# Optimization experiments

Hardware: AMD Instinct MI355X
Metric: run time of the kernel (lower is better)

The kernel has to match this reference:

```python
import math
import jax, jax.numpy as jnp
import numpy as np

B, C, T = 4, 512, 1024
H = 8
KC = C // H
WIN = 4


def _get_relative_embeddings(emb, length):
    win = (emb.shape[1] - 1) // 2
    pad_length = max(length - (win + 1), 0)
    slice_start = max(win + 1 - length, 0)
    slice_end = slice_start + 2 * length - 1
    if pad_length > 0:
        emb = jnp.pad(emb, ((0, 0), (pad_length, pad_length), (0, 0)))
    return emb[:, slice_start:slice_end]


def _relative_to_absolute(x):
    # x: [b, h, L, 2L-1] -> [b, h, L, L] via skew trick
    b, h, L, _ = x.shape
    x = jnp.pad(x, ((0, 0), (0, 0), (0, 0), (0, 1)))          # [b,h,L,2L]
    x_flat = x.reshape(b, h, L * 2 * L)
    x_flat = jnp.pad(x_flat, ((0, 0), (0, 0), (0, L - 1)))    # [b,h,(L+1)(2L-1)]
    x_final = x_flat.reshape(b, h, L + 1, 2 * L - 1)
    return x_final[:, :, :L, L - 1:]


def _absolute_to_relative(x):
    # x: [b, h, L, L] -> [b, h, L, 2L-1]
    b, h, L, _ = x.shape
    x = jnp.pad(x, ((0, 0), (0, 0), (0, 0), (0, L - 1)))      # [b,h,L,2L-1]
    x_flat = x.reshape(b, h, L * (2 * L - 1))
    x_flat = jnp.pad(x_flat, ((0, 0), (0, 0), (L, 0)))        # [b,h,2L^2]
    x_final = x_flat.reshape(b, h, L, 2 * L)
    return x_final[:, :, :, 1:]


def setup_inputs() -> dict:
    key = jax.random.key(0)
    ks = jax.random.split(key, 12)
    xavier = math.sqrt(6.0 / (C + C))  # xavier_uniform for [C, C, 1] conv weight
    rel_std = KC ** (-0.5)
    return {
        "x": jax.random.normal(ks[0], (B, C, T), dtype=jnp.float32),
        "wq": jax.random.uniform(ks[1], (C, C), jnp.float32, -xavier, xavier),
        "bq": jnp.zeros((C,), jnp.float32),
        "wk": jax.random.uniform(ks[2], (C, C), jnp.float32, -xavier, xavier),
        "bk": jnp.zeros((C,), jnp.float32),
        "wv": jax.random.uniform(ks[3], (C, C), jnp.float32, -xavier, xavier),
        "bv": jnp.zeros((C,), jnp.float32),
        "wo": jax.random.normal(ks[4], (C, C), jnp.float32) * (1.0 / math.sqrt(C)),
        "bo": jnp.zeros((C,), jnp.float32),
        "emb_rel_k": jax.random.normal(ks[5], (1, 2 * WIN + 1, KC), jnp.float32) * rel_std,
        "emb_rel_v": jax.random.normal(ks[6], (1, 2 * WIN + 1, KC), jnp.float32) * rel_std,
    }


def reference(x, wq, bq, wk, bk, wv, bv, wo, bo, emb_rel_k, emb_rel_v):
    b, c, t = x.shape
    # 1x1 conv == channel matmul
    q = jnp.einsum("oi,bit->bot", wq, x) + bq[:, None]
    k = jnp.einsum("oi,bit->bot", wk, x) + bk[:, None]
    v = jnp.einsum("oi,bit->bot", wv, x) + bv[:, None]
    # [b, H, t, kc]
    q = q.reshape(b, H, KC, t).transpose(0, 1, 3, 2)
    k = k.reshape(b, H, KC, t).transpose(0, 1, 3, 2)
    v = v.reshape(b, H, KC, t).transpose(0, 1, 3, 2)
    inv_sqrt = 1.0 / math.sqrt(KC)
    scores = jnp.einsum("bhtc,bhsc->bhts", q, k) * inv_sqrt
    rel_k = _get_relative_embeddings(emb_rel_k, t)[0]            # [2t-1, kc]
    rel_logits = jnp.einsum("bhtc,rc->bhtr", q, rel_k)           # [b,h,t,2t-1]
    scores = scores + _relative_to_absolute(rel_logits) * inv_sqrt
    p_attn = jax.nn.softmax(scores, axis=-1)
    output = jnp.einsum("bhts,bhsc->bhtc", p_attn, v)
    rel_weights = _absolute_to_relative(p_attn)                  # [b,h,t,2t-1]
    rel_v = _get_relative_embeddings(emb_rel_v, t)[0]            # [2t-1, kc]
    output = output + jnp.einsum("bhtr,rc->bhtc", rel_weights, rel_v)
    output = output.transpose(0, 1, 3, 2).reshape(b, c, t)
    return jnp.einsum("oi,bit->bot", wo, output) + bo[:, None]
```

## Files before the change

### kernel.cpp

```cpp
#include <hip/hip_runtime.h>
#include <hip/hip_bf16.h>

#define Bdim 4
#define Cdim 512
#define Tdim 1024
#define Hn   8
#define KCd  64

#define QK_SCALE 0.18033688011112042f

typedef __attribute__((ext_vector_type(8))) short bf16x8;
typedef __attribute__((ext_vector_type(4))) float f32x4;

__device__ __forceinline__ unsigned short f2bf(float f) {
    __hip_bfloat16 h = __float2bfloat16(f);
    return *reinterpret_cast<unsigned short*>(&h);
}
__device__ __forceinline__ float bf16_f32(unsigned short h) {
    return __uint_as_float(((unsigned)h) << 16);
}
__device__ __forceinline__ void split8(const float* f, bf16x8& h8, bf16x8& l8) {
    #pragma unroll
    for (int e = 0; e < 8; ++e) {
        const unsigned short hh = f2bf(f[e]);
        h8[e] = (short)hh;
        l8[e] = (short)f2bf(f[e] - bf16_f32(hh));
    }
}
__device__ __forceinline__ float max3f(float a, float b, float c) {
    return fmaxf(fmaxf(a, b), c);
}

__device__ __forceinline__ int sw(int row, int col) {
    return (row << 6) + ((((col >> 3) ^ (row & 7)) << 3) | (col & 7));
}
__device__ __forceinline__ bf16x8 fragld(const unsigned short* a, int row, int kstep, int quad) {
    return *(const bf16x8*)&a[(row << 6) + ((((kstep << 2) | quad) ^ (row & 7)) << 3)];
}


__global__ __launch_bounds__(256) void prep_kernel(
    const float* __restrict__ wq, const float* __restrict__ wk,
    const float* __restrict__ wv, const float* __restrict__ wo,
    const float* __restrict__ x,
    unsigned short* __restrict__ WAhi, unsigned short* __restrict__ WAlo,
    unsigned short* __restrict__ XBhi, unsigned short* __restrict__ XBlo)
{
    const int w = threadIdx.x >> 6, lane = threadIdx.x & 63;
    const int l15 = lane & 15, quad = lane >> 4;
    const int task = blockIdx.x * 4 + w;

    if (task < 2048) {
        const int mtile = task >> 4, kt = task & 15;
        const int sel = mtile >> 5;
        const float* W = sel == 0 ? wq : (sel == 1 ? wk : (sel == 2 ? wv : wo));
        const int row = (mtile & 31) * 16 + l15;
        const float* p = W + (size_t)row * Cdim + kt * 32 + quad * 8;
        float f[8];
        *(float4*)&f[0] = *(const float4*)p;
        *(float4*)&f[4] = *(const float4*)(p + 4);
        bf16x8 h8, l8;
        split8(f, h8, l8);
        const size_t base = (size_t)task * 512 + lane * 8;
        *(bf16x8*)(WAhi + base) = h8;
        *(bf16x8*)(WAlo + base) = l8;
    } else {
        const int t2 = task - 2048;
        const int b = t2 >> 10, ntile = (t2 >> 4) & 63, kt = t2 & 15;
        const float* Xb = x + (size_t)b * Cdim * Tdim;
        const int n = ntile * 16 + l15;
        const int k0 = kt * 32 + quad * 8;
        float f[8];
        #pragma unroll
        for (int e = 0; e < 8; ++e) f[e] = Xb[(size_t)(k0 + e) * Tdim + n];
        bf16x8 h8, l8;
        split8(f, h8, l8);
        const size_t base = (size_t)t2 * 512 + lane * 8;
        *(bf16x8*)(XBhi + base) = h8;
        *(bf16x8*)(XBlo + base) = l8;
    }
}

__global__ __launch_bounds__(256, 3) void gemm_qkv(
    const unsigned short* __restrict__ Ahi, const unsigned short* __restrict__ Alo,
    const unsigned short* __restrict__ Bhi, const unsigned short* __restrict__ Blo,
    const float* __restrict__ bq, const float* __restrict__ bk, const float* __restrict__ bv,
    unsigned short* __restrict__ qhi, unsigned short* __restrict__ qlo,
    unsigned short* __restrict__ khi, unsigned short* __restrict__ klo,
    unsigned short* __restrict__ vhi, unsigned short* __restrict__ vlo)
{
    __shared__ alignas(16) unsigned short As[2][4][2][512];

    const int tid = threadIdx.x;
    const int w = tid >> 6, lane = tid & 63;
    const int l15 = lane & 15, quad = lane >> 4;
    const int lo8 = lane << 3;

    const int id = blockIdx.x;
    const int xcd = id & 7, slot = id >> 3;
    const int m64 = slot >> 2;
    const int col128 = xcd * 4 + (slot & 3);
    const int col = col128 * 4 + w;
    const int b = col >> 5, n32 = col & 31;
    const int sel = m64 >> 3;
    const int mtb = m64 * 4;
    const int ntb = b * 64 + n32 * 2;

    const unsigned short* Asrc_h = Ahi + (size_t)(mtb + w) * 8192 + lo8;
    const unsigned short* Asrc_l = Alo + (size_t)(mtb + w) * 8192 + lo8;

    f32x4 acc[4][2];
    #pragma unroll
    for (int i = 0; i < 4; ++i)
        #pragma unroll
        for (int j = 0; j < 2; ++j) acc[i][j] = (f32x4){0.f, 0.f, 0.f, 0.f};

    bf16x8 Bh[2][2], Bl[2][2];
    #pragma unroll
    for (int nt = 0; nt < 2; ++nt) {
        const size_t o = (size_t)(ntb + nt) * 8192 + lo8;
        Bh[0][nt] = *(const bf16x8*)(Bhi + o);
        Bl[0][nt] = *(const bf16x8*)(Blo + o);
    }
    *(bf16x8*)&As[0][w][0][lo8] = *(const bf16x8*)Asrc_h;
    *(bf16x8*)&As[0][w][1][lo8] = *(const bf16x8*)Asrc_l;
    __syncthreads();

    for (int kt = 0; kt < 16; ++kt) {
        const int cur = kt & 1, nxt = cur ^ 1;
        bf16x8 stgh, stgl;
        if (kt < 15) {
            const int kn = (kt + 1) * 512;
            stgh = *(const bf16x8*)(Asrc_h + kn);
            stgl = *(const bf16x8*)(Asrc_l + kn);
            #pragma unroll
            for (int nt = 0; nt < 2; ++nt) {
                const size_t o = (size_t)(ntb + nt) * 8192 + kn + lo8;
                Bh[nxt][nt] = *(const bf16x8*)(Bhi + o);
                Bl[nxt][nt] = *(const bf16x8*)(Blo + o);
            }
        }
        bf16x8 Afh[4], Afl[4];
        #pragma unroll
        for (int mt = 0; mt < 4; ++mt) {
            Afh[mt] = *(const bf16x8*)&As[cur][mt][0][lo8];
            Afl[mt] = *(const bf16x8*)&As[cur][mt][1][lo8];
        }
        #pragma unroll
        for (int mt = 0; mt < 4; ++mt)
            #pragma unroll
            for (int nt = 0; nt < 2; ++nt) {
                f32x4 c = acc[mt][nt];
                c = __builtin_amdgcn_mfma_f32_16x16x32_bf16(Afh[mt], Bh[cur][nt], c, 0, 0, 0);
                c = __builtin_amdgcn_mfma_f32_16x16x32_bf16(Afh[mt], Bl[cur][nt], c, 0, 0, 0);
                c = __builtin_amdgcn_mfma_f32_16x16x32_bf16(Afl[mt], Bh[cur][nt], c, 0, 0, 0);
                acc[mt][nt] = c;
            }
        if (kt < 15) {
            *(bf16x8*)&As[nxt][w][0][lo8] = stgh;
            *(bf16x8*)&As[nxt][w][1][lo8] = stgl;
        }
        __syncthreads();
    }

    const int head = m64 & 7;
    const size_t hbase = ((size_t)(b * Hn + head) * 16) << 12;
    if (sel < 2) {
        const float* Bv = sel == 0 ? bq : bk;
        unsigned short* ph = sel == 0 ? qhi : khi;
        unsigned short* pl = sel == 0 ? qlo : klo;
        const float qscale = sel == 0 ? QK_SCALE : 1.0f;
        #pragma unroll
        for (int mt = 0; mt < 4; ++mt) {
            const int c0 = mt * 16 + quad * 4;
            float bb[4];
            #pragma unroll
            for (int r = 0; r < 4; ++r) bb[r] = Bv[head * 64 + c0 + r];
            const int lane_out = (((c0 >> 3) & 3) << 4) + l15;
            const int e0 = c0 & 7;
            const int cg = c0 >> 5;
            #pragma unroll
            for (int nt = 0; nt < 2; ++nt) {
                const int tile = n32 >> 1;
                const int rhi = (n32 & 1) * 2 + nt;
                const int g = rhi * 2 + cg;
                const size_t off = hbase + ((size_t)tile << 12) + g * 512
                                 + (size_t)lane_out * 8 + e0;
                ushort4 h4, l4;
                #pragma unroll
                for (int r = 0; r < 4; ++r) {
                    const float v = (acc[mt][nt][r] + bb[r]) * qscale;
                    const unsigned short hh = f2bf(v);
                    ((unsigned short*)&h4)[r] = hh;
                    ((unsigned short*)&l4)[r] = f2bf(v - bf16_f32(hh));
                }
                *(ushort4*)(ph + off) = h4;
                *(ushort4*)(pl + off) = l4;
            }
        }
    } else {
        #pragma unroll
        for (int mt = 0; mt < 4; ++mt) {
            const int c0 = mt * 16 + quad * 4;
            float bb[4];
            #pragma unroll
            for (int r = 0; r < 4; ++r) bb[r] = bv[head * 64 + c0 + r];
            #pragma unroll
            for (int nt = 0; nt < 2; ++nt) {
                const int t = n32 * 32 + nt * 16 + l15;
                const int tile = t >> 6, jl = t & 63;
                const int jg = jl >> 5, lanej = ((jl >> 3) & 3) << 4;
                const int e = jl & 7;
                const size_t tb = hbase + ((size_t)tile << 12);
                #pragma unroll
                for (int r = 0; r < 4; ++r) {
                    const int c = c0 + r;
                    const int g = mt * 2 + jg;
                    const int lane_v = lanej + (c & 15);
                    const float v = acc[mt][nt][r] + bb[r];
                    const unsigned short hh = f2bf(v);
                    const size_t off = tb + g * 512 + (size_t)lane_v * 8 + e;
                    vhi[off] = hh;
                    vlo[off] = f2bf(v - bf16_f32(hh));
                }
            }
        }
    }
}

__global__ __launch_bounds__(256) void gemm_out(
    const unsigned short* __restrict__ Ahi, const unsigned short* __restrict__ Alo,
    const unsigned short* __restrict__ Bhi, const unsigned short* __restrict__ Blo,
    const float* __restrict__ bo, float* __restrict__ out)
{
    __shared__ alignas(16) unsigned short Bs[2][2][2][512];

    const int tid = threadIdx.x;
    const int w = tid >> 6, lane = tid & 63;
    const int l15 = lane & 15, quad = lane >> 4;
    const int lo8 = lane << 3;

    const int id = blockIdx.x;
    const int xcd = id & 7, slot = id >> 3;
    const int col = xcd * 16 + (slot >> 2);
    const int mg  = slot & 3;
    const int b = col >> 5, n32 = col & 31;
    const int m32 = mg * 4 + w;
    const int mtb = 96 + m32 * 2;
    const int ntb = b * 64 + n32 * 2;

    const unsigned short* Bsrc =
        ((w & 1) ? Blo : Bhi) + (size_t)(ntb + (w >> 1)) * 8192 + lo8;

    f32x4 acc[2][2];
    #pragma unroll
    for (int i = 0; i < 2; ++i)
        #pragma unroll
        for (int j = 0; j < 2; ++j) acc[i][j] = (f32x4){0.f, 0.f, 0.f, 0.f};

    bf16x8 Ah[2][2], Al[2][2];
    #pragma unroll
    for (int mt = 0; mt < 2; ++mt) {
        const size_t o = (size_t)(mtb + mt) * 8192 + lo8;
        Ah[0][mt] = *(const bf16x8*)(Ahi + o);
        Al[0][mt] = *(const bf16x8*)(Alo + o);
    }
    *(bf16x8*)&Bs[0][w >> 1][w & 1][lo8] = *(const bf16x8*)Bsrc;
    __syncthreads();

    for (int kt = 0; kt < 16; ++kt) {
        const int cur = kt & 1, nxt = cur ^ 1;
        bf16x8 stg;
        if (kt < 15) {
            const int kn = (kt + 1) * 512;
            stg = *(const bf16x8*)(Bsrc + kn);
            #pragma unroll
            for (int mt = 0; mt < 2; ++mt) {
                const size_t o = (size_t)(mtb + mt) * 8192 + kn + lo8;
                Ah[nxt][mt] = *(const bf16x8*)(Ahi + o);
                Al[nxt][mt] = *(const bf16x8*)(Alo + o);
            }
        }
        bf16x8 Bfh[2], Bfl[2];
        #pragma unroll
        for (int nt = 0; nt < 2; ++nt) {
            Bfh[nt] = *(const bf16x8*)&Bs[cur][nt][0][lo8];
            Bfl[nt] = *(const bf16x8*)&Bs[cur][nt][1][lo8];
        }
        #pragma unroll
        for (int mt = 0; mt < 2; ++mt)
            #pragma unroll
            for (int nt = 0; nt < 2; ++nt) {
                f32x4 c = acc[mt][nt];
                c = __builtin_amdgcn_mfma_f32_16x16x32_bf16(Ah[cur][mt], Bfh[nt], c, 0, 0, 0);
                c = __builtin_amdgcn_mfma_f32_16x16x32_bf16(Ah[cur][mt], Bfl[nt], c, 0, 0, 0);
                c = __builtin_amdgcn_mfma_f32_16x16x32_bf16(Al[cur][mt], Bfh[nt], c, 0, 0, 0);
                acc[mt][nt] = c;
            }
        if (kt < 15) {
            *(bf16x8*)&Bs[nxt][w >> 1][w & 1][lo8] = stg;
        }
        __syncthreads();
    }

    float* Ob = out + (size_t)b * Cdim * Tdim;
    #pragma unroll
    for (int mt = 0; mt < 2; ++mt) {
        const int m = m32 * 32 + mt * 16 + quad * 4;
        float bb[4];
        #pragma unroll
        for (int r = 0; r < 4; ++r) bb[r] = bo[m + r];
        #pragma unroll
        for (int nt = 0; nt < 2; ++nt) {
            const int t = n32 * 32 + nt * 16 + l15;
            #pragma unroll
            for (int r = 0; r < 4; ++r)
                Ob[(size_t)(m + r) * Tdim + t] = acc[mt][nt][r] + bb[r];
        }
    }
}

__global__ __launch_bounds__(256) void attn_mfma(
    const unsigned short* __restrict__ qhi, const unsigned short* __restrict__ qlo,
    const unsigned short* __restrict__ khi, const unsigned short* __restrict__ klo,
    const unsigned short* __restrict__ vhi, const unsigned short* __restrict__ vlo,
    const float* __restrict__ ek,
    const float* __restrict__ ev,
    unsigned short* __restrict__ cxhi, unsigned short* __restrict__ cxlo)
{
    __shared__ alignas(16) unsigned short psh[4096], psl[4096];
    __shared__ float rk[576];
    __shared__ float evs[576];
    __shared__ float bandp[576];

    const int tid = threadIdx.x;
    int it, h, b;
    {
        const int n = blockIdx.x;
        const int xcd = n & 7, slot = n >> 3;
        const int pair = (xcd << 2) | (slot >> 4);
        it = slot & 15;
        b = pair >> 3;
        h = pair & 7;
    }
    const int i0 = it * 64;
    const int lane = tid & 63, w = tid >> 6;
    const int l15 = lane & 15, quad = lane >> 4;
    const int m_blk = w * 16 + l15;
    const int lo8 = lane << 3;

    const size_t bh16 = (size_t)(b * Hn + h) * 16;

    bf16x8 qfh[2], qfl[2];
    {
        const unsigned short* qth = qhi + ((bh16 + it) << 12);
        const unsigned short* qtl = qlo + ((bh16 + it) << 12);
        #pragma unroll
        for (int ks = 0; ks < 2; ++ks) {
            qfh[ks] = *(const bf16x8*)(qth + (((w << 1) | ks) << 9) + lo8);
            qfl[ks] = *(const bf16x8*)(qtl + (((w << 1) | ks) << 9) + lo8);
        }
    }

    bf16x8 ekh[2], ekl[2];
    #pragma unroll
    for (int ks = 0; ks < 2; ++ks) {
        #pragma unroll
        for (int j = 0; j < 8; ++j) { ekh[ks][j] = 0; ekl[ks][j] = 0; }
        if (l15 < 9) {
            #pragma unroll
            for (int j = 0; j < 8; ++j) {
                const float v = ek[l15 * 64 + ks * 32 + quad * 8 + j];
                const unsigned short hh = f2bf(v);
                ekh[ks][j] = (short)hh;
                ekl[ks][j] = (short)f2bf(v - bf16_f32(hh));
            }
        }
    }

    {
        f32x4 rkD = (f32x4){0.f, 0.f, 0.f, 0.f};
        #pragma unroll
        for (int ks = 0; ks < 2; ++ks) {
            rkD = __builtin_amdgcn_mfma_f32_16x16x32_bf16(qfh[ks], ekh[ks], rkD, 0, 0, 0);
            rkD = __builtin_amdgcn_mfma_f32_16x16x32_bf16(qfh[ks], ekl[ks], rkD, 0, 0, 0);
            rkD = __builtin_amdgcn_mfma_f32_16x16x32_bf16(qfl[ks], ekh[ks], rkD, 0, 0, 0);
        }
        if (l15 < 9) {
            #pragma unroll
            for (int r = 0; r < 4; ++r)
                rk[(w * 16 + quad * 4 + r) * 9 + l15] = rkD[r];
        }
    }
    for (int idx = tid; idx < 576; idx += 256) evs[idx] = ev[idx];
    __syncthreads();

    int osw[4];
    #pragma unroll
    for (int jt = 0; jt < 4; ++jt) osw[jt] = sw(m_blk, jt * 16 + quad * 4);

    float m_run = -1e30f, l_run = 0.f;
    f32x4 Oc[4];
    #pragma unroll
    for (int ct = 0; ct < 4; ++ct) Oc[ct] = (f32x4){0.f, 0.f, 0.f, 0.f};

    const unsigned short* kh0 = khi + (bh16 << 12);
    const unsigned short* kl0 = klo + (bh16 << 12);
    const unsigned short* vh0 = vhi + (bh16 << 12);
    const unsigned short* vl0 = vlo + (bh16 << 12);

    for (int t = 0; t < 16; ++t) {
        const int j0 = t << 6;
        const size_t tb = (size_t)t << 12;
        const unsigned short* kht = kh0 + tb;
        const unsigned short* klt = kl0 + tb;
        const unsigned short* vht = vh0 + tb;
        const unsigned short* vlt = vl0 + tb;

        bf16x8 vbh[2][4], vbl[2][4];
        #pragma unroll
        for (int ks = 0; ks < 2; ++ks)
            #pragma unroll
            for (int ct = 0; ct < 4; ++ct) {
                vbh[ks][ct] = *(const bf16x8*)(vht + (((ct << 1) | ks) << 9) + lo8);
                vbl[ks][ct] = *(const bf16x8*)(vlt + (((ct << 1) | ks) << 9) + lo8);
            }

        f32x4 Sc[4];
        #pragma unroll
        for (int jt = 0; jt < 4; ++jt) Sc[jt] = (f32x4){0.f, 0.f, 0.f, 0.f};
        #pragma unroll
        for (int ks = 0; ks < 2; ++ks) {
            bf16x8 ah[4], al[4];
            #pragma unroll
            for (int jt = 0; jt < 4; ++jt) {
                ah[jt] = *(const bf16x8*)(kht + (((jt << 1) | ks) << 9) + lo8);
                al[jt] = *(const bf16x8*)(klt + (((jt << 1) | ks) << 9) + lo8);
            }
            #pragma unroll
            for (int jt = 0; jt < 4; ++jt) {
                Sc[jt] = __builtin_amdgcn_mfma_f32_16x16x32_bf16(ah[jt], qfh[ks], Sc[jt], 0, 0, 0);
                Sc[jt] = __builtin_amdgcn_mfma_f32_16x16x32_bf16(ah[jt], qfl[ks], Sc[jt], 0, 0, 0);
                Sc[jt] = __builtin_amdgcn_mfma_f32_16x16x32_bf16(al[jt], qfh[ks], Sc[jt], 0, 0, 0);
            }
        }

        const int dt = j0 - i0;
        const bool diag = (dt >= -67 && dt <= 67);
        if (diag) {
            #pragma unroll
            for (int jt = 0; jt < 4; ++jt) {
                const int db = dt + jt * 16 + quad * 4 - m_blk;
                #pragma unroll
                for (int r = 0; r < 4; ++r) {
                    const int d = db + r;
                    if ((unsigned)(d + 4) <= 8u) Sc[jt][r] += rk[m_blk * 9 + d + 4];
                }
            }
        }

        const float t0m = max3f(Sc[0][0], Sc[0][1], Sc[0][2]);
        const float t1m = max3f(Sc[0][3], Sc[1][0], Sc[1][1]);
        const float t2m = max3f(Sc[1][2], Sc[1][3], Sc[2][0]);
        const float t3m = max3f(Sc[2][1], Sc[2][2], Sc[2][3]);
        const float t4m = max3f(Sc[3][0], Sc[3][1], Sc[3][2]);
        const float mt = fmaxf(max3f(t0m, t1m, t2m), max3f(t3m, t4m, Sc[3][3]));
        float mr = fmaxf(mt, __shfl_xor(mt, 16));
        mr = fmaxf(mr, __shfl_xor(mr, 32));

        if (__any(mr > m_run)) {
            const float mn = fmaxf(m_run, mr);
            const float alpha = __builtin_amdgcn_exp2f(m_run - mn);
            m_run = mn;
            l_run *= alpha;
            const float al0 = __shfl(alpha, quad * 4 + 0);
            const float al1 = __shfl(alpha, quad * 4 + 1);
            const float al2 = __shfl(alpha, quad * 4 + 2);
            const float al3 = __shfl(alpha, quad * 4 + 3);
            #pragma unroll
            for (int ct = 0; ct < 4; ++ct) {
                Oc[ct][0] *= al0; Oc[ct][1] *= al1; Oc[ct][2] *= al2; Oc[ct][3] *= al3;
            }
        }

        #pragma unroll
        for (int jt = 0; jt < 4; ++jt)
            #pragma unroll
            for (int r = 0; r < 4; ++r)
                Sc[jt][r] = __builtin_amdgcn_exp2f(Sc[jt][r] - m_run);

        float rs = ((Sc[0][0] + Sc[0][1]) + (Sc[0][2] + Sc[0][3]))
                 + ((Sc[1][0] + Sc[1][1]) + (Sc[1][2] + Sc[1][3]))
                 + ((Sc[2][0] + Sc[2][1]) + (Sc[2][2] + Sc[2][3]))
                 + ((Sc[3][0] + Sc[3][1]) + (Sc[3][2] + Sc[3][3]));
        rs += __shfl_xor(rs, 16);
        rs += __shfl_xor(rs, 32);
        l_run += rs;

        if (diag) {
            #pragma unroll
            for (int jt = 0; jt < 4; ++jt) {
                const int db = dt + jt * 16 + quad * 4 - m_blk;
                #pragma unroll
                for (int r = 0; r < 4; ++r) {
                    const int d = db + r;
                    if ((unsigned)(d + 4) <= 8u) bandp[m_blk * 9 + d + 4] = Sc[jt][r];
                }
            }
        }

        #pragma unroll
        for (int jt = 0; jt < 4; ++jt) {
            ushort4 ph, pl;
            ph.x = f2bf(Sc[jt][0]); pl.x = f2bf(Sc[jt][0] - bf16_f32(ph.x));
            ph.y = f2bf(Sc[jt][1]); pl.y = f2bf(Sc[jt][1] - bf16_f32(ph.y));
            ph.z = f2bf(Sc[jt][2]); pl.z = f2bf(Sc[jt][2] - bf16_f32(ph.z));
            ph.w = f2bf(Sc[jt][3]); pl.w = f2bf(Sc[jt][3] - bf16_f32(ph.w));
            *(ushort4*)&psh[osw[jt]] = ph;
            *(ushort4*)&psl[osw[jt]] = pl;
        }

        #pragma unroll
        for (int ks = 0; ks < 2; ++ks) {
            bf16x8 pah = fragld(psh, m_blk, ks, quad);
            bf16x8 pal = fragld(psl, m_blk, ks, quad);
            #pragma unroll
            for (int ct = 0; ct < 4; ++ct) {
                Oc[ct] = __builtin_amdgcn_mfma_f32_16x16x32_bf16(pah, vbh[ks][ct], Oc[ct], 0, 0, 0);
                Oc[ct] = __builtin_amdgcn_mfma_f32_16x16x32_bf16(pah, vbl[ks][ct], Oc[ct], 0, 0, 0);
                Oc[ct] = __builtin_amdgcn_mfma_f32_16x16x32_bf16(pal, vbh[ks][ct], Oc[ct], 0, 0, 0);
            }
        }

        if (diag) {
            #pragma unroll
            for (int r = 0; r < 4; ++r) {
                const int mrow = w * 16 + quad * 4 + r;
                const int ig = i0 + mrow;
                #pragma unroll
                for (int e = 0; e < 9; ++e) {
                    const int jl = ig + e - 4 - j0;
                    if ((unsigned)jl < 64u) {
                        const float p = bandp[mrow * 9 + e];
                        #pragma unroll
                        for (int ct = 0; ct < 4; ++ct)
                            Oc[ct][r] += p * evs[e * 64 + ct * 16 + l15];
                    }
                }
            }
        }
    }

    const float rlv = 1.f / l_run;
    float rl[4];
    rl[0] = __shfl(rlv, quad * 4 + 0);
    rl[1] = __shfl(rlv, quad * 4 + 1);
    rl[2] = __shfl(rlv, quad * 4 + 2);
    rl[3] = __shfl(rlv, quad * 4 + 3);
    const int ntile16 = it * 4 + w;
    const int e = l15 & 7;
    #pragma unroll
    for (int ct = 0; ct < 4; ++ct) {
        const int cl = ct * 16 + l15;
        const int ktc = h * 2 + (cl >> 5);
        const int lane_c = (((ct * 2 + (l15 >> 3)) & 3) << 4) + quad * 4;
        const size_t base = (((size_t)(b * 64 + ntile16)) * 16 + ktc) * 512;
        #pragma unroll
        for (int r = 0; r < 4; ++r) {
            const float v = Oc[ct][r] * rl[r];
            const unsigned short hh = f2bf(v);
            const size_t off = base + (size_t)(lane_c + r) * 8 + e;
            cxhi[off] = hh;
            cxlo[off] = f2bf(v - bf16_f32(hh));
        }
    }
}

extern "C" void kernel_launch(void* const* d_in, const int* in_sizes, int n_in,
                              void* d_out, int out_size, void* d_ws, size_t ws_size,
                              hipStream_t stream) {
    const float* x  = (const float*)d_in[0];
    const float* wq = (const float*)d_in[1];
    const float* bq = (const float*)d_in[2];
    const float* wk = (const float*)d_in[3];
    const float* bk = (const float*)d_in[4];
    const float* wv = (const float*)d_in[5];
    const float* bv = (const float*)d_in[6];
    const float* wo = (const float*)d_in[7];
    const float* bo = (const float*)d_in[8];
    const float* ek = (const float*)d_in[9];
    const float* ev = (const float*)d_in[10];
    float* out = (float*)d_out;

    const size_t PW = 2048u * 512u;
    const size_t PX = 4u * 1024u * 512u;
    unsigned short* WAhi = (unsigned short*)d_ws;
    unsigned short* WAlo = WAhi + PW;
    unsigned short* XBhi = WAlo + PW;
    unsigned short* XBlo = XBhi + PX;
    unsigned short* qhi  = XBlo + PX;
    unsigned short* qlo  = qhi + PX;
    unsigned short* khi  = qlo + PX;
    unsigned short* klo  = khi + PX;
    unsigned short* vhi  = klo + PX;
    unsigned short* vlo  = vhi + PX;
    unsigned short* cxhi = vlo + PX;
    unsigned short* cxlo = cxhi + PX;

    prep_kernel<<<dim3(1536), 256, 0, stream>>>(
        wq, wk, wv, wo, x, WAhi, WAlo, XBhi, XBlo);

    gemm_qkv<<<dim3(768), 256, 0, stream>>>(
        WAhi, WAlo, XBhi, XBlo, bq, bk, bv,
        qhi, qlo, khi, klo, vhi, vlo);

    attn_mfma<<<dim3(512), 256, 0, stream>>>(
        qhi, qlo, khi, klo, vhi, vlo, ek, ev, cxhi, cxlo);

    gemm_out<<<dim3(512), 256, 0, stream>>>(
        WAhi, WAlo, cxhi, cxlo, bo, out);
}
```

Before: 161.1 us.

## Stage x transpose through LDS and share A/B tiles in output GEMM

The prep kernel now loads 32x32 tiles of x with coalesced float4 reads into padded shared memory and transposes there, replacing strided per-element global loads. Each wave handles two n-tiles, so the grid shrinks. The output GEMM now stages both the weight (A) and context (B) hi/lo fragments in shared memory with a 2x2 wave arrangement over a 64x64 block tile, so A tiles are shared across waves instead of each wave loading its own A from global memory. This adds more LDS traffic and staging registers per thread.

```diff
diff --git a/kernel.cpp b/kernel.cpp
--- a/kernel.cpp
+++ b/kernel.cpp
@@ -46,6 +46,8 @@
     unsigned short* __restrict__ WAhi, unsigned short* __restrict__ WAlo,
     unsigned short* __restrict__ XBhi, unsigned short* __restrict__ XBlo)
 {
+    __shared__ float Xl[4][32][33];
+
     const int w = threadIdx.x >> 6, lane = threadIdx.x & 63;
     const int l15 = lane & 15, quad = lane >> 4;
     const int task = blockIdx.x * 4 + w;
@@ -66,18 +68,33 @@
         *(bf16x8*)(WAlo + base) = l8;
     } else {
         const int t2 = task - 2048;
-        const int b = t2 >> 10, ntile = (t2 >> 4) & 63, kt = t2 & 15;
+        const int b = t2 >> 9, np = (t2 >> 4) & 31, kt = t2 & 15;
         const float* Xb = x + (size_t)b * Cdim * Tdim;
-        const int n = ntile * 16 + l15;
-        const int k0 = kt * 32 + quad * 8;
-        float f[8];
-        #pragma unroll
-        for (int e = 0; e < 8; ++e) f[e] = Xb[(size_t)(k0 + e) * Tdim + n];
-        bf16x8 h8, l8;
-        split8(f, h8, l8);
-        const size_t base = (size_t)t2 * 512 + lane * 8;
-        *(bf16x8*)(XBhi + base) = h8;
-        *(bf16x8*)(XBlo + base) = l8;
+        const int k0 = kt * 32;
+        const int n0 = np * 32;
+
+        {
+            const int row = lane & 31, ch = lane >> 5;
+            const float* src = Xb + (size_t)(k0 + row) * Tdim + n0 + ch * 16;
+            float* dst = &Xl[w][row][ch * 16];
+            *(float4*)(dst + 0)  = *(const float4*)(src + 0);
+            *(float4*)(dst + 4)  = *(const float4*)(src + 4);
+            *(float4*)(dst + 8)  = *(const float4*)(src + 8);
+            *(float4*)(dst + 12) = *(const float4*)(src + 12);
+        }
+
+        #pragma unroll
+        for (int j = 0; j < 2; ++j) {
+            float f[8];
+            #pragma unroll
+            for (int e = 0; e < 8; ++e) f[e] = Xl[w][quad * 8 + e][j * 16 + l15];
+            bf16x8 h8, l8;
+            split8(f, h8, l8);
+            const int ntile = np * 2 + j;
+            const size_t base = ((size_t)(b * 1024 + ntile * 16 + kt)) * 512 + lane * 8;
+            *(bf16x8*)(XBhi + base) = h8;
+            *(bf16x8*)(XBlo + base) = l8;
+        }
     }
 }
 
@@ -233,7 +250,7 @@
     const unsigned short* __restrict__ Bhi, const unsigned short* __restrict__ Blo,
     const float* __restrict__ bo, float* __restrict__ out)
 {
-    __shared__ alignas(16) unsigned short Bs[2][2][2][512];
+    __shared__ alignas(16) unsigned short St[2][16][512];
 
     const int tid = threadIdx.x;
     const int w = tid >> 6, lane = tid & 63;
@@ -242,15 +259,27 @@
 
     const int id = blockIdx.x;
     const int xcd = id & 7, slot = id >> 3;
-    const int col = xcd * 16 + (slot >> 2);
-    const int mg  = slot & 3;
-    const int b = col >> 5, n32 = col & 31;
-    const int m32 = mg * 4 + w;
-    const int mtb = 96 + m32 * 2;
-    const int ntb = b * 64 + n32 * 2;
-
-    const unsigned short* Bsrc =
-        ((w & 1) ? Blo : Bhi) + (size_t)(ntb + (w >> 1)) * 8192 + lo8;
+    const int ncol64 = xcd * 8 + (slot >> 3);
+    const int mg8 = slot & 7;
+    const int wr = w >> 1, wc = w & 1;
+    const int m32 = mg8 * 2 + wr;
+    const int n32g = ncol64 * 2 + wc;
+    const int b = n32g >> 5, n32 = n32g & 31;
+    const int nb = (ncol64 & 15) * 4;
+    const int bb64 = (ncol64 >> 4) * 64;
+
+    const unsigned short* csrc[4];
+    #pragma unroll
+    for (int i = 0; i < 4; ++i) {
+        const int c = w * 4 + i;
+        if (c < 8) {
+            const int mt = c >> 1;
+            csrc[i] = ((c & 1) ? Alo : Ahi) + (size_t)(96 + mg8 * 4 + mt) * 8192 + lo8;
+        } else {
+            const int nt = (c - 8) >> 1;
+            csrc[i] = ((c & 1) ? Blo : Bhi) + (size_t)(bb64 + nb + nt) * 8192 + lo8;
+        }
+    }
 
     f32x4 acc[2][2];
     #pragma unroll
@@ -258,47 +287,44 @@
         #pragma unroll
         for (int j = 0; j < 2; ++j) acc[i][j] = (f32x4){0.f, 0.f, 0.f, 0.f};
 
-    bf16x8 Ah[2][2], Al[2][2];
-    #pragma unroll
-    for (int mt = 0; mt < 2; ++mt) {
-        const size_t o = (size_t)(mtb + mt) * 8192 + lo8;
-        Ah[0][mt] = *(const bf16x8*)(Ahi + o);
-        Al[0][mt] = *(const bf16x8*)(Alo + o);
-    }
-    *(bf16x8*)&Bs[0][w >> 1][w & 1][lo8] = *(const bf16x8*)Bsrc;
+    #pragma unroll
+    for (int i = 0; i < 4; ++i)
+        *(bf16x8*)&St[0][w * 4 + i][lo8] = *(const bf16x8*)csrc[i];
     __syncthreads();
 
     for (int kt = 0; kt < 16; ++kt) {
         const int cur = kt & 1, nxt = cur ^ 1;
-        bf16x8 stg;
+        bf16x8 stg[4];
         if (kt < 15) {
             const int kn = (kt + 1) * 512;
-            stg = *(const bf16x8*)(Bsrc + kn);
-            #pragma unroll
-            for (int mt = 0; mt < 2; ++mt) {
-                const size_t o = (size_t)(mtb + mt) * 8192 + kn + lo8;
-                Ah[nxt][mt] = *(const bf16x8*)(Ahi + o);
-                Al[nxt][mt] = *(const bf16x8*)(Alo + o);
-            }
-        }
-        bf16x8 Bfh[2], Bfl[2];
-        #pragma unroll
-        for (int nt = 0; nt < 2; ++nt) {
-            Bfh[nt] = *(const bf16x8*)&Bs[cur][nt][0][lo8];
-            Bfl[nt] = *(const bf16x8*)&Bs[cur][nt][1][lo8];
+            #pragma unroll
+            for (int i = 0; i < 4; ++i)
+                stg[i] = *(const bf16x8*)(csrc[i] + kn);
+        }
+        bf16x8 Afh[2], Afl[2], Bfh[2], Bfl[2];
+        #pragma unroll
+        for (int i = 0; i < 2; ++i) {
+            const int lm = wr * 2 + i;
+            Afh[i] = *(const bf16x8*)&St[cur][lm * 2 + 0][lo8];
+            Afl[i] = *(const bf16x8*)&St[cur][lm * 2 + 1][lo8];
+            const int ln = wc * 2 + i;
+            Bfh[i] = *(const bf16x8*)&St[cur][8 + ln * 2 + 0][lo8];
+            Bfl[i] = *(const bf16x8*)&St[cur][8 + ln * 2 + 1][lo8];
         }
         #pragma unroll
         for (int mt = 0; mt < 2; ++mt)
             #pragma unroll
             for (int nt = 0; nt < 2; ++nt) {
                 f32x4 c = acc[mt][nt];
-                c = __builtin_amdgcn_mfma_f32_16x16x32_bf16(Ah[cur][mt], Bfh[nt], c, 0, 0, 0);
-                c = __builtin_amdgcn_mfma_f32_16x16x32_bf16(Ah[cur][mt], Bfl[nt], c, 0, 0, 0);
-                c = __builtin_amdgcn_mfma_f32_16x16x32_bf16(Al[cur][mt], Bfh[nt], c, 0, 0, 0);
+                c = __builtin_amdgcn_mfma_f32_16x16x32_bf16(Afh[mt], Bfh[nt], c, 0, 0, 0);
+                c = __builtin_amdgcn_mfma_f32_16x16x32_bf16(Afh[mt], Bfl[nt], c, 0, 0, 0);
+                c = __builtin_amdgcn_mfma_f32_16x16x32_bf16(Afl[mt], Bfh[nt], c, 0, 0, 0);
                 acc[mt][nt] = c;
             }
         if (kt < 15) {
-            *(bf16x8*)&Bs[nxt][w >> 1][w & 1][lo8] = stg;
+            #pragma unroll
+            for (int i = 0; i < 4; ++i)
+                *(bf16x8*)&St[nxt][w * 4 + i][lo8] = stg[i];
         }
         __syncthreads();
     }
@@ -607,7 +633,7 @@
     unsigned short* cxhi = vlo + PX;
     unsigned short* cxlo = cxhi + PX;
 
-    prep_kernel<<<dim3(1536), 256, 0, stream>>>(
+    prep_kernel<<<dim3(1024), 256, 0, stream>>>(
         wq, wk, wv, wo, x, WAhi, WAlo, XBhi, XBlo);
 
     gemm_qkv<<<dim3(768), 256, 0, stream>>>(
```

Measured after the change: 160.5 us, median of 5. About the same (-0.4%).
